# Kernel optimization log

Hardware: AMD Instinct MI355X
Metric: run time of the kernel (lower is better)

Reference implementation:

```python
import jax, jax.numpy as jnp
import numpy as np

ALPHA, GAMMA = 0.25, 2.0            # focal loss params (cfg defaults)
W_CLASS, W_BBOX, W_GIOU = 2.0, 5.0, 2.0
N_CANDIDATE_K = 5                   # top-k ious used to derive dynamic k
CENTER_RADIUS = 2.5
B, Q, G, C = 32, 2000, 64, 80
IMG_W, IMG_H = 1333.0, 800.0


def _box_iou(a, b):
    # a: [Q,4] xyxy, b: [G,4] xyxy -> iou [Q,G], union [Q,G]
    area_a = (a[:, 2] - a[:, 0]) * (a[:, 3] - a[:, 1])
    area_b = (b[:, 2] - b[:, 0]) * (b[:, 3] - b[:, 1])
    lt = jnp.maximum(a[:, None, :2], b[None, :, :2])
    rb = jnp.minimum(a[:, None, 2:], b[None, :, 2:])
    wh = jnp.clip(rb - lt, 0.0)
    inter = wh[..., 0] * wh[..., 1]
    union = area_a[:, None] + area_b[None, :] - inter
    return inter / union, union


def _generalized_box_iou(a, b):
    iou, union = _box_iou(a, b)
    lt = jnp.minimum(a[:, None, :2], b[None, :, :2])
    rb = jnp.maximum(a[:, None, 2:], b[None, :, 2:])
    wh = jnp.clip(rb - lt, 0.0)
    area_c = wh[..., 0] * wh[..., 1]
    return iou - (area_c - union) / area_c


def _get_in_boxes_info(boxes, gt):
    # boxes, gt: absolute xyxy. Anchor centers inside gt box / inside center region.
    cx = (boxes[:, 0] + boxes[:, 2]) * 0.5
    cy = (boxes[:, 1] + boxes[:, 3]) * 0.5
    is_in_boxes = ((cx[:, None] > gt[None, :, 0]) & (cx[:, None] < gt[None, :, 2]) &
                   (cy[:, None] > gt[None, :, 1]) & (cy[:, None] < gt[None, :, 3]))
    gt_cx = (gt[:, 0] + gt[:, 2]) * 0.5
    gt_cy = (gt[:, 1] + gt[:, 3]) * 0.5
    gt_w = gt[:, 2] - gt[:, 0]
    gt_h = gt[:, 3] - gt[:, 1]
    is_in_centers = ((cx[:, None] > (gt_cx - CENTER_RADIUS * gt_w)[None, :]) &
                     (cx[:, None] < (gt_cx + CENTER_RADIUS * gt_w)[None, :]) &
                     (cy[:, None] > (gt_cy - CENTER_RADIUS * gt_h)[None, :]) &
                     (cy[:, None] < (gt_cy + CENTER_RADIUS * gt_h)[None, :]))
    fg_mask = is_in_boxes.any(1) | is_in_centers.any(1)
    return fg_mask, is_in_boxes & is_in_centers


def _dedup(cost, matching):
    # queries matched to >1 gt keep only their min-cost gt
    over = matching.sum(1) > 1
    keep = jax.nn.one_hot(jnp.argmin(cost, axis=1), cost.shape[1], dtype=matching.dtype)
    return jnp.where(over[:, None], keep, matching)


def _dynamic_k_matching(cost, ious):
    Qn, Gn = cost.shape
    topk_ious = jax.lax.top_k(ious.T, N_CANDIDATE_K)[0]              # [G,k]
    dynamic_ks = jnp.maximum(topk_ious.sum(1).astype(jnp.int32), 1)  # [G]
    # rank of each query within each gt's cost column (ascending)
    ranks = jnp.argsort(jnp.argsort(cost, axis=0), axis=0)
    matching = (ranks < dynamic_ks[None, :]).astype(cost.dtype)      # [Q,G]
    matching = _dedup(cost, matching)

    # ensure every gt gets >=1 query; bounded loop replaces data-dependent while
    def body(_, carry):
        cost_c, match_c = carry
        unmatched = match_c.sum(0) == 0                              # [G]
        any_un = unmatched.any()
        matched_q = match_c.sum(1) > 0
        cost_n = cost_c + jnp.where(matched_q, 1e5, 0.0)[:, None]
        add = jax.nn.one_hot(jnp.argmin(cost_n, axis=0), Qn, dtype=match_c.dtype).T
        match_n = jnp.maximum(match_c, add * unmatched[None, :].astype(match_c.dtype))
        match_n = _dedup(cost_n, match_n)
        return (jnp.where(any_un, cost_n, cost_c), jnp.where(any_un, match_n, match_c))

    cost, matching = jax.lax.fori_loop(0, Gn, body, (cost, matching))
    masked = jnp.where(matching > 0, cost, jnp.inf)
    matched_query_id = jnp.argmin(masked, axis=0)                    # [G]
    return matching, matched_query_id


def _match_one(logits, boxes, tgt_ids, gt_boxes, size_out, size_tgt):
    fg_mask, in_bc = _get_in_boxes_info(boxes, gt_boxes)
    ious, _ = _box_iou(boxes, gt_boxes)                              # [Q,G]
    neg = (1.0 - ALPHA) * logits ** GAMMA * (-jnp.log(1.0 - logits + 1e-8))
    pos = ALPHA * (1.0 - logits) ** GAMMA * (-jnp.log(logits + 1e-8))
    cost_class = jnp.take(pos - neg, tgt_ids, axis=1)                # [Q,G]
    out_n = boxes / size_out                                         # [Q,4]
    tgt_n = gt_boxes / size_tgt                                      # [G,4]
    cost_bbox = jnp.abs(out_n[:, None, :] - tgt_n[None, :, :]).sum(-1)  # L1 cdist
    cost_giou = -_generalized_box_iou(boxes, gt_boxes)
    cost = (W_BBOX * cost_bbox + W_CLASS * cost_class + W_GIOU * cost_giou
            + 100.0 * (~in_bc).astype(cost_bbox.dtype))
    cost = cost + jnp.where(fg_mask, 0.0, 1e4)[:, None]
    return _dynamic_k_matching(cost, ious)


def _rand_boxes(key, n_shape):
    k1, k2 = jax.random.split(key)
    wh = jnp.array([IMG_W, IMG_H], jnp.float32)
    ctr = jax.random.uniform(k1, n_shape + (2,)) * wh
    size = jax.random.uniform(k2, n_shape + (2,)) * (wh * 0.3) + 8.0
    x1y1 = jnp.clip(ctr - size * 0.5, 0.0, wh)
    x2y2 = jnp.clip(ctr + size * 0.5, 0.0, wh)
    x2y2 = jnp.maximum(x2y2, x1y1 + 1.0)
    return jnp.concatenate([x1y1, x2y2], axis=-1)


def setup_inputs() -> dict:
    key = jax.random.key(0)
    k1, k2, k3, k4 = jax.random.split(key, 4)
    pred_logits = jax.random.uniform(k1, (B, Q, C), minval=1e-4, maxval=1.0 - 1e-4)
    pred_boxes = _rand_boxes(k2, (B, Q))
    gt_classes = jax.random.randint(k3, (B, G), 0, C)
    gt_boxes = _rand_boxes(k4, (B, G))
    sz = jnp.array([IMG_W, IMG_H, IMG_W, IMG_H], jnp.float32)
    return {
        'pred_logits': pred_logits,
        'pred_boxes': pred_boxes,
        'gt_classes': gt_classes,
        'gt_boxes': gt_boxes,
        'image_size_xyxy': jnp.tile(sz, (B, 1)),
        'image_size_xyxy_tgt': jnp.tile(sz, (B, G, 1)),
    }


def reference(pred_logits, pred_boxes, gt_classes, gt_boxes, image_size_xyxy, image_size_xyxy_tgt):
    # matching: [B,Q,G] 0/1 assignment matrix (row q matched to gt g);
    # matched_query_id: [B,G] best query per gt. Padded-G, fixed-shape analog of
    # the per-image variable-length (indices, matched_ids) lists.
    matching, matched_query_id = jax.vmap(_match_one)(
        pred_logits, pred_boxes, gt_classes, gt_boxes, image_size_xyxy, image_size_xyxy_tgt)
    return matching, matched_query_id
```

## Files before the change

### kernel.cpp

```cpp
#include <hip/hip_runtime.h>
#include <cmath>

#pragma clang fp contract(off)

#define BB 32
#define QQ 2000
#define GG 64
#define CCH 80
#define TOPC 16

__global__ __launch_bounds__(256) void cost_kernel(
    const float* __restrict__ logits, const float* __restrict__ boxes,
    const int* __restrict__ gtc, const float* __restrict__ gtb,
    const float* __restrict__ szout, const float* __restrict__ sztgt,
    float* __restrict__ cost, int* __restrict__ rowarg,
    float* __restrict__ out_match) {
#pragma clang fp contract(off)
  const int b = blockIdx.y;
  const int q0 = blockIdx.x * 64;
  const int t = threadIdx.x;
  const int w = t >> 6, lane = t & 63;

  __shared__ float4 s_qb[64];
  __shared__ float s_tile[64 * 65];

  const int gbase = (b * GG + lane) * 4;
  const float g0 = gtb[gbase + 0], g1 = gtb[gbase + 1];
  const float g2 = gtb[gbase + 2], g3 = gtb[gbase + 3];
  const float t0 = g0 / sztgt[gbase + 0], t1 = g1 / sztgt[gbase + 1];
  const float t2 = g2 / sztgt[gbase + 2], t3 = g3 / sztgt[gbase + 3];
  const float garea = (g2 - g0) * (g3 - g1);
  const float gcx = (g0 + g2) * 0.5f, gcy = (g1 + g3) * 0.5f;
  const float gw = g2 - g0, gh = g3 - g1;
  const float cxlo = gcx - 2.5f * gw, cxhi = gcx + 2.5f * gw;
  const float cylo = gcy - 2.5f * gh, cyhi = gcy + 2.5f * gh;
  const int cls = gtc[b * GG + lane];
  const float so0 = szout[b * 4 + 0], so1 = szout[b * 4 + 1];
  const float so2 = szout[b * 4 + 2], so3 = szout[b * 4 + 3];

  if (t < 64) {
    int q = q0 + t;
    s_qb[t] = (q < QQ) ? reinterpret_cast<const float4*>(boxes)[b * QQ + q]
                       : make_float4(0.f, 0.f, 1.f, 1.f);
  }
  __syncthreads();

  const float* lbase = logits + (size_t)b * QQ * CCH;
  for (int i = 0; i < 16; ++i) {
    const int qi = w * 16 + i;
    const int q = q0 + qi;
    float4 bx = s_qb[qi];
    float x1 = bx.x, y1 = bx.y, x2 = bx.z, y2 = bx.w;
    float on0 = x1 / so0, on1 = y1 / so1, on2 = x2 / so2, on3 = y2 / so3;
    float cx = (x1 + x2) * 0.5f, cy = (y1 + y2) * 0.5f;
    float areaa = (x2 - x1) * (y2 - y1);

    bool ib = (cx > g0) & (cx < g2) & (cy > g1) & (cy < g3);
    bool ic = (cx > cxlo) & (cx < cxhi) & (cy > cylo) & (cy < cyhi);
    bool fg = (__ballot(ib) != 0ull) || (__ballot(ic) != 0ull);
    float fgadd = fg ? 0.0f : 1e4f;

    float ltx = fmaxf(x1, g0), lty = fmaxf(y1, g1);
    float rbx = fminf(x2, g2), rby = fminf(y2, g3);
    float iw = fmaxf(rbx - ltx, 0.0f), ih = fmaxf(rby - lty, 0.0f);
    float inter = iw * ih;
    float uni = (areaa + garea) - inter;
    float iou = inter / uni;
    float ex1 = fminf(x1, g0), ey1 = fminf(y1, g1);
    float ex2 = fmaxf(x2, g2), ey2 = fmaxf(y2, g3);
    float ew = fmaxf(ex2 - ex1, 0.0f), eh = fmaxf(ey2 - ey1, 0.0f);
    float areac = ew * eh;
    float giou = iou - (areac - uni) / areac;

    float p = (q < QQ) ? lbase[(size_t)q * CCH + cls] : 0.5f;
    float negc = (0.75f * (p * p)) * (-logf((1.0f - p) + 1e-8f));
    float posc = (0.25f * ((1.0f - p) * (1.0f - p))) * (-logf(p + 1e-8f));
    float ccls = posc - negc;

    float cb = ((fabsf(on0 - t0) + fabsf(on1 - t1)) + fabsf(on2 - t2)) + fabsf(on3 - t3);
    float notbc = (ib & ic) ? 0.0f : 1.0f;
    float c = ((5.0f * cb + 2.0f * ccls) + 2.0f * (-giou)) + 100.0f * notbc;
    c = c + fgadd;

    s_tile[qi * 65 + lane] = c;

    float bv = c; int bg = lane;
    for (int off = 32; off; off >>= 1) {
      float ov = __shfl_down(bv, off, 64); int og = __shfl_down(bg, off, 64);
      if (ov < bv || (ov == bv && og < bg)) { bv = ov; bg = og; }
    }
    if (lane == 0 && q < QQ) rowarg[b * QQ + q] = bg;
  }
  __syncthreads();

  float* cb_out = cost + (size_t)b * GG * QQ;
  const int qi = t & 63;
  const int q = q0 + qi;
  if (q < QQ) {
    #pragma unroll
    for (int pass = 0; pass < 16; ++pass) {
      int g = (t >> 6) + pass * 4;
      cb_out[(size_t)g * QQ + q] = s_tile[qi * 65 + g];
    }
  }

  int nq = QQ - q0; if (nq > 64) nq = 64;
  if (nq > 0) {
    float4* zb = reinterpret_cast<float4*>(out_match + ((size_t)b * QQ + q0) * GG);
    int n4 = nq * GG / 4;
    float4 z = make_float4(0.f, 0.f, 0.f, 0.f);
    for (int i = t; i < n4; i += 256) zb[i] = z;
  }
}

__global__ __launch_bounds__(256) void pick_kernel(
    const float* __restrict__ boxes, const float* __restrict__ gtb,
    const float* __restrict__ cost, short* __restrict__ lists,
    int* __restrict__ dynks) {
#pragma clang fp contract(off)
  const int gwave = blockIdx.x * 4 + (threadIdx.x >> 6);
  const int lane = threadIdx.x & 63;
  const int b = gwave >> 6, col = gwave & 63;

  const int gbase = (b * GG + col) * 4;
  const float gx1 = gtb[gbase + 0], gy1 = gtb[gbase + 1];
  const float gx2 = gtb[gbase + 2], gy2 = gtb[gbase + 3];
  const float ga = (gx2 - gx1) * (gy2 - gy1);

  float v[32];
  #pragma unroll
  for (int j = 0; j < 32; ++j) {
    int q = lane + (j << 6);
    if (q < QQ) {
      float4 bx = reinterpret_cast<const float4*>(boxes)[b * QQ + q];
      float areaa = (bx.z - bx.x) * (bx.w - bx.y);
      float ltx = fmaxf(bx.x, gx1), lty = fmaxf(bx.y, gy1);
      float rbx = fminf(bx.z, gx2), rby = fminf(bx.w, gy2);
      float iw = fmaxf(rbx - ltx, 0.0f), ih = fmaxf(rby - lty, 0.0f);
      float inter = iw * ih;
      v[j] = inter / ((areaa + ga) - inter);
    } else v[j] = -1.0f;
  }
  unsigned rm = 0u;
  float s = 0.0f;
  for (int pass = 0; pass < 5; ++pass) {
    float bv = -1e30f; int bq = 0x7fffffff;
    #pragma unroll
    for (int j = 0; j < 32; ++j) {
      int q = lane + (j << 6);
      if (q < QQ && !((rm >> j) & 1u) && v[j] > bv) { bv = v[j]; bq = q; }
    }
    for (int off = 32; off; off >>= 1) {
      float ov = __shfl_down(bv, off, 64); int oq = __shfl_down(bq, off, 64);
      if (ov > bv || (ov == bv && oq < bq)) { bv = ov; bq = oq; }
    }
    bv = __shfl(bv, 0, 64); bq = __shfl(bq, 0, 64);
    s += bv;
    if ((bq & 63) == lane) rm |= (1u << (bq >> 6));
  }
  int dynk = (int)s;
  if (dynk < 1) dynk = 1;
  if (lane == 0) dynks[b * GG + col] = dynk;

  const float* ccol = cost + (size_t)(b * GG + col) * QQ;
  #pragma unroll
  for (int j = 0; j < 32; ++j) {
    int q = lane + (j << 6);
    v[j] = (q < QQ) ? ccol[q] : 0.0f;
  }
  rm = 0u;
  for (int pass = 0; pass < TOPC; ++pass) {
    float bv = INFINITY; int bq = 0x7fffffff;
    #pragma unroll
    for (int j = 0; j < 32; ++j) {
      int q = lane + (j << 6);
      if (q < QQ && !((rm >> j) & 1u) && v[j] < bv) { bv = v[j]; bq = q; }
    }
    for (int off = 32; off; off >>= 1) {
      float ov = __shfl_down(bv, off, 64); int oq = __shfl_down(bq, off, 64);
      if (ov < bv || (ov == bv && oq < bq)) { bv = ov; bq = oq; }
    }
    bq = __shfl(bq, 0, 64);
    if (lane == 0) lists[(b * GG + col) * TOPC + pass] = (short)bq;
    if ((bq & 63) == lane) rm |= (1u << (bq >> 6));
  }
}

__global__ __launch_bounds__(256) void serial_kernel(
    const float* __restrict__ cost, const short* __restrict__ lists,
    const int* __restrict__ dynks, const int* __restrict__ rowarg,
    float* __restrict__ out_match, float* __restrict__ out_ids) {
#pragma clang fp contract(off)
  const int b = blockIdx.x;
  const int tid = threadIdx.x;

  __shared__ unsigned s_mlo[QQ], s_mhi[QQ];
  __shared__ int s_first[QQ];
  __shared__ int s_pushed[QQ];
  __shared__ short s_rarg[QQ];
  __shared__ short s_list[GG * TOPC];
  __shared__ int s_cnt[GG];
  __shared__ short s_chosen[GG];
  __shared__ unsigned long long s_pack[GG];
  __shared__ int s_added[GG];
  __shared__ short s_ucols[GG];
  __shared__ short s_fb[GG];
  __shared__ int s_nadd, s_nfb, s_Tv;

  for (int q = tid; q < QQ; q += 256) {
    s_mlo[q] = 0u; s_mhi[q] = 0u; s_first[q] = -1; s_pushed[q] = -1;
    s_rarg[q] = (short)rowarg[b * QQ + q];
  }
  for (int i = tid; i < GG * TOPC; i += 256) s_list[i] = lists[b * GG * TOPC + i];
  if (tid < GG) s_cnt[tid] = 0;
  __syncthreads();

  if (tid < GG) {
    int dynk = dynks[b * GG + tid];
    s_cnt[tid] = dynk;
    for (int i = 0; i < dynk; ++i) {
      int q = s_list[tid * TOPC + i];
      if (tid < 32) atomicOr(&s_mlo[q], 1u << tid);
      else          atomicOr(&s_mhi[q], 1u << (tid - 32));
      s_first[q] = 0;
    }
  }
  __syncthreads();

  for (int q = tid; q < QQ; q += 256) {
    unsigned lo = s_mlo[q], hi = s_mhi[q];
    if (__popc(lo) + __popc(hi) > 1) {
      int bg = s_rarg[q];
      unsigned tl = lo, th = hi;
      while (tl) { int g = __ffs(tl) - 1; tl &= tl - 1; if (g != bg) atomicSub(&s_cnt[g], 1); }
      while (th) { int g = __ffs(th) + 31; th &= th - 1; if (g != bg) atomicSub(&s_cnt[g], 1); }
      bool had = (bg < 32) ? ((lo >> bg) & 1u) : ((hi >> (bg - 32)) & 1u);
      if (!had) atomicAdd(&s_cnt[bg], 1);
      s_mlo[q] = (bg < 32) ? (1u << bg) : 0u;
      s_mhi[q] = (bg >= 32) ? (1u << (bg - 32)) : 0u;
    }
  }
  __syncthreads();

  const float* costb = cost + (size_t)b * GG * QQ;

  if (tid < 64) {
    const int lane = tid;
    int T = 0;
    for (int iter = 0; iter < GG; ++iter) {
      unsigned long long bal = __ballot(s_cnt[lane] > 0);
      unsigned long long um = ~bal;
      if (um == 0ull) break;
      T++;

      bool isun = (um >> lane) & 1ull;
      int nu = __popcll(um);
      int pos = __popcll(um & ((1ull << lane) - 1ull));
      if (isun) s_ucols[pos] = (short)lane;
      if (lane == 0) { s_nfb = 0; s_nadd = 0; }

      const int sg = lane >> 4, li = lane & 15;
      for (int base = 0; base < nu; base += 4) {
        int ci = base + sg;
        int col = (ci < nu) ? (int)s_ucols[ci] : -1;
        bool cand_un = false; int cq = 0;
        if (col >= 0) {
          cq = s_list[col * TOPC + li];
          cand_un = ((s_mlo[cq] | s_mhi[cq]) == 0u);
        }
        unsigned long long bb = __ballot(cand_un);
        unsigned sub = (unsigned)((bb >> (sg * 16)) & 0xFFFFull);
        if (col >= 0) {
          if (sub) {
            if (li == __ffs(sub) - 1) s_chosen[col] = (short)cq;
          } else if (li == 0) {
            int slot = atomicAdd(&s_nfb, 1);
            s_fb[slot] = (short)col;
          }
        }
      }

      int nfb = s_nfb;
      for (int fi = 0; fi < nfb; ++fi) {
        int col = s_fb[fi];
        const float* ccol = costb + (size_t)col * QQ;
        float bv = INFINITY; int bq = 0x7fffffff;
        for (int q2 = lane; q2 < QQ; q2 += 64) {
          if ((s_mlo[q2] | s_mhi[q2]) == 0u) {
            float cv = ccol[q2];
            if (cv < bv) { bv = cv; bq = q2; }
          }
        }
        for (int off = 32; off; off >>= 1) {
          float ov = __shfl_down(bv, off, 64); int oq = __shfl_down(bq, off, 64);
          if (ov < bv || (ov == bv && oq < bq)) { bv = ov; bq = oq; }
        }
        bq = __shfl(bq, 0, 64);
        if (bq == 0x7fffffff) {
          bv = INFINITY; bq = 0x7fffffff;
          for (int q2 = lane; q2 < QQ; q2 += 64) {
            float cv = ccol[q2];
            int k = (s_first[q2] >= 0) ? (iter + 1 - s_first[q2]) : 0;
            for (int tt = 0; tt < k; ++tt) cv += 1e5f;
            if (cv < bv) { bv = cv; bq = q2; }
          }
          for (int off = 32; off; off >>= 1) {
            float ov = __shfl_down(bv, off, 64); int oq = __shfl_down(bq, off, 64);
            if (ov < bv || (ov == bv && oq < bq)) { bv = ov; bq = oq; }
          }
          bq = __shfl(bq, 0, 64);
        }
        if (lane == 0) s_chosen[col] = (short)bq;
      }

      if (isun) {
        int q = s_chosen[lane];
        if (lane < 32) atomicOr(&s_mlo[q], 1u << lane);
        else           atomicOr(&s_mhi[q], 1u << (lane - 32));
        atomicAdd(&s_cnt[lane], 1);
        if (s_first[q] == -1) s_first[q] = iter + 1;
        if (atomicExch(&s_pushed[q], iter) != iter) {
          int slot = atomicAdd(&s_nadd, 1);
          s_added[slot] = q;
        }
      }

      int na = s_nadd;
      if (lane < na) {
        int q = s_added[lane];
        unsigned lo = s_mlo[q], hi = s_mhi[q];
        if (__popc(lo) + __popc(hi) > 1) {
          int bg = s_rarg[q];
          unsigned tl = lo, th = hi;
          while (tl) { int g = __ffs(tl) - 1; tl &= tl - 1; if (g != bg) atomicSub(&s_cnt[g], 1); }
          while (th) { int g = __ffs(th) + 31; th &= th - 1; if (g != bg) atomicSub(&s_cnt[g], 1); }
          bool had = (bg < 32) ? ((lo >> bg) & 1u) : ((hi >> (bg - 32)) & 1u);
          if (!had) atomicAdd(&s_cnt[bg], 1);
          s_mlo[q] = (bg < 32) ? (1u << bg) : 0u;
          s_mhi[q] = (bg >= 32) ? (1u << (bg - 32)) : 0u;
        }
      }
    }
    if (tid == 0) s_Tv = T;
  }
  __syncthreads();
  const int T = s_Tv;

  if (tid < GG) s_pack[tid] = 0xFFFFFFFFFFFFFFFFull;
  __syncthreads();
  for (int q = tid; q < QQ; q += 256) {
    unsigned lo = s_mlo[q], hi = s_mhi[q];
    if (lo | hi) {
      int g = lo ? (__ffs(lo) - 1) : (__ffs(hi) + 31);
      float cv = costb[(size_t)g * QQ + q];
      int k = T - s_first[q];
      for (int tt = 0; tt < k; ++tt) cv += 1e5f;
      unsigned ub = __float_as_uint(cv);
      ub = (ub & 0x80000000u) ? ~ub : (ub | 0x80000000u);
      unsigned long long pk = ((unsigned long long)ub << 16) | (unsigned)q;
      atomicMin(&s_pack[g], pk);
    }
  }
  __syncthreads();
  if (tid < GG) {
    unsigned long long pk = s_pack[tid];
    out_ids[b * GG + tid] =
        (pk == 0xFFFFFFFFFFFFFFFFull) ? 0.0f : (float)(pk & 0xFFFFull);
  }
  for (int q = tid; q < QQ; q += 256) {
    unsigned lo = s_mlo[q], hi = s_mhi[q];
    if (lo | hi) {
      int g = lo ? (__ffs(lo) - 1) : (__ffs(hi) + 31);
      out_match[((size_t)b * QQ + q) * GG + g] = 1.0f;
    }
  }
}

extern "C" void kernel_launch(void* const* d_in, const int* in_sizes, int n_in,
                              void* d_out, int out_size, void* d_ws, size_t ws_size,
                              hipStream_t stream) {
  const float* logits = (const float*)d_in[0];
  const float* boxes  = (const float*)d_in[1];
  const int*   gtc    = (const int*)d_in[2];
  const float* gtbx   = (const float*)d_in[3];
  const float* szout  = (const float*)d_in[4];
  const float* sztgt  = (const float*)d_in[5];
  float* out = (float*)d_out;

  const size_t matchN  = (size_t)BB * QQ * GG;
  const size_t rowargN = (size_t)BB * QQ;
  const size_t listsN  = (size_t)BB * GG * TOPC;
  const size_t dynksN  = (size_t)BB * GG;

  char* p = (char*)d_ws;
  float* cost   = (float*)p;          p += matchN * 4;
  int*   rowarg = (int*)p;            p += rowargN * 4;
  short* lists  = (short*)p;          p += listsN * 2;
  int*   dynks  = (int*)p;

  float* out_ids = out + matchN;

  hipLaunchKernelGGL(cost_kernel, dim3(32, BB), dim3(256), 0, stream,
                     logits, boxes, gtc, gtbx, szout, sztgt, cost, rowarg, out);
  hipLaunchKernelGGL(pick_kernel, dim3(BB * GG / 4), dim3(256), 0, stream,
                     boxes, gtbx, cost, lists, dynks);
  hipLaunchKernelGGL(serial_kernel, dim3(BB), dim3(256), 0, stream,
                     cost, lists, dynks, rowarg, out, out_ids);
}
```

Before: 147.5 us.

## Split each pick column across a 256-thread block instead of one wave

The pick kernel now gives each (batch, gt) column a full 256-thread block rather than a single 64-lane wave. Each thread holds 8 values instead of 32, and the per-pass argmax/argmin combines the four waves' results through shared memory with a __syncthreads. Picked entries are overwritten with sentinels rather than tracked in a bitmask. This shortens the serial per-pass scan and uses more parallelism, but adds a block barrier to each of 21 passes and launches four times as many blocks.

```diff
diff --git a/kernel.cpp b/kernel.cpp
--- a/kernel.cpp
+++ b/kernel.cpp
@@ -118,19 +118,23 @@
     const float* __restrict__ cost, short* __restrict__ lists,
     int* __restrict__ dynks) {
 #pragma clang fp contract(off)
-  const int gwave = blockIdx.x * 4 + (threadIdx.x >> 6);
-  const int lane = threadIdx.x & 63;
-  const int b = gwave >> 6, col = gwave & 63;
+  const int bc = blockIdx.x;
+  const int b = bc >> 6, col = bc & 63;
+  const int tid = threadIdx.x;
+  const int w = tid >> 6, lane = tid & 63;
+
+  __shared__ float s_wv[5 + TOPC][4];
+  __shared__ int   s_wi[5 + TOPC][4];
 
   const int gbase = (b * GG + col) * 4;
   const float gx1 = gtb[gbase + 0], gy1 = gtb[gbase + 1];
   const float gx2 = gtb[gbase + 2], gy2 = gtb[gbase + 3];
   const float ga = (gx2 - gx1) * (gy2 - gy1);
 
-  float v[32];
+  float v[8];
   #pragma unroll
-  for (int j = 0; j < 32; ++j) {
-    int q = lane + (j << 6);
+  for (int j = 0; j < 8; ++j) {
+    int q = tid + (j << 8);
     if (q < QQ) {
       float4 bx = reinterpret_cast<const float4*>(boxes)[b * QQ + q];
       float areaa = (bx.z - bx.x) * (bx.w - bx.y);
@@ -139,50 +143,60 @@
       float iw = fmaxf(rbx - ltx, 0.0f), ih = fmaxf(rby - lty, 0.0f);
       float inter = iw * ih;
       v[j] = inter / ((areaa + ga) - inter);
-    } else v[j] = -1.0f;
-  }
-  unsigned rm = 0u;
+    } else v[j] = -1e30f;
+  }
   float s = 0.0f;
   for (int pass = 0; pass < 5; ++pass) {
     float bv = -1e30f; int bq = 0x7fffffff;
     #pragma unroll
-    for (int j = 0; j < 32; ++j) {
-      int q = lane + (j << 6);
-      if (q < QQ && !((rm >> j) & 1u) && v[j] > bv) { bv = v[j]; bq = q; }
+    for (int j = 0; j < 8; ++j) {
+      if (v[j] > bv) { bv = v[j]; bq = tid + (j << 8); }
     }
     for (int off = 32; off; off >>= 1) {
       float ov = __shfl_down(bv, off, 64); int oq = __shfl_down(bq, off, 64);
       if (ov > bv || (ov == bv && oq < bq)) { bv = ov; bq = oq; }
     }
-    bv = __shfl(bv, 0, 64); bq = __shfl(bq, 0, 64);
+    if (lane == 0) { s_wv[pass][w] = bv; s_wi[pass][w] = bq; }
+    __syncthreads();
+    bv = s_wv[pass][0]; bq = s_wi[pass][0];
+    #pragma unroll
+    for (int i = 1; i < 4; ++i) {
+      float ov = s_wv[pass][i]; int oq = s_wi[pass][i];
+      if (ov > bv || (ov == bv && oq < bq)) { bv = ov; bq = oq; }
+    }
     s += bv;
-    if ((bq & 63) == lane) rm |= (1u << (bq >> 6));
+    if ((bq & 255) == tid) v[bq >> 8] = -1e30f;
   }
   int dynk = (int)s;
   if (dynk < 1) dynk = 1;
-  if (lane == 0) dynks[b * GG + col] = dynk;
+  if (tid == 0) dynks[b * GG + col] = dynk;
 
   const float* ccol = cost + (size_t)(b * GG + col) * QQ;
   #pragma unroll
-  for (int j = 0; j < 32; ++j) {
-    int q = lane + (j << 6);
-    v[j] = (q < QQ) ? ccol[q] : 0.0f;
-  }
-  rm = 0u;
+  for (int j = 0; j < 8; ++j) {
+    int q = tid + (j << 8);
+    v[j] = (q < QQ) ? ccol[q] : INFINITY;
+  }
   for (int pass = 0; pass < TOPC; ++pass) {
     float bv = INFINITY; int bq = 0x7fffffff;
     #pragma unroll
-    for (int j = 0; j < 32; ++j) {
-      int q = lane + (j << 6);
-      if (q < QQ && !((rm >> j) & 1u) && v[j] < bv) { bv = v[j]; bq = q; }
+    for (int j = 0; j < 8; ++j) {
+      if (v[j] < bv) { bv = v[j]; bq = tid + (j << 8); }
     }
     for (int off = 32; off; off >>= 1) {
       float ov = __shfl_down(bv, off, 64); int oq = __shfl_down(bq, off, 64);
       if (ov < bv || (ov == bv && oq < bq)) { bv = ov; bq = oq; }
     }
-    bq = __shfl(bq, 0, 64);
-    if (lane == 0) lists[(b * GG + col) * TOPC + pass] = (short)bq;
-    if ((bq & 63) == lane) rm |= (1u << (bq >> 6));
+    if (lane == 0) { s_wv[5 + pass][w] = bv; s_wi[5 + pass][w] = bq; }
+    __syncthreads();
+    bv = s_wv[5 + pass][0]; bq = s_wi[5 + pass][0];
+    #pragma unroll
+    for (int i = 1; i < 4; ++i) {
+      float ov = s_wv[5 + pass][i]; int oq = s_wi[5 + pass][i];
+      if (ov < bv || (ov == bv && oq < bq)) { bv = ov; bq = oq; }
+    }
+    if (tid == 0) lists[(b * GG + col) * TOPC + pass] = (short)bq;
+    if ((bq & 255) == tid) v[bq >> 8] = INFINITY;
   }
 }
 
@@ -402,7 +416,7 @@
 
   hipLaunchKernelGGL(cost_kernel, dim3(32, BB), dim3(256), 0, stream,
                      logits, boxes, gtc, gtbx, szout, sztgt, cost, rowarg, out);
-  hipLaunchKernelGGL(pick_kernel, dim3(BB * GG / 4), dim3(256), 0, stream,
+  hipLaunchKernelGGL(pick_kernel, dim3(BB * GG), dim3(256), 0, stream,
                      boxes, gtbx, cost, lists, dynks);
   hipLaunchKernelGGL(serial_kernel, dim3(BB), dim3(256), 0, stream,
                      cost, lists, dynks, rowarg, out, out_ids);
```

New measurement: 159.4 us. 8.0% more time.
